# Kernel optimization log

Hardware: AMD Instinct MI355X
Metric: run time of the kernel (lower is better)

## Reference

```python
import jax, jax.numpy as jnp
import numpy as np

EPS = 1e-8
NEG_INF = -jnp.inf


def setup_inputs() -> dict:
    key = jax.random.key(0)
    k1, k2, k3, k4 = jax.random.split(key, 4)
    B1, S1, B2, S2, H = 64, 128, 64, 128, 768
    x1 = jax.random.normal(k1, (B1, S1, H), dtype=jnp.float32)
    x2 = jax.random.normal(k2, (B2, S2, H), dtype=jnp.float32)
    mask1 = jax.random.randint(k3, (B1, S1), 0, 2).astype(jnp.int32)
    mask2 = jax.random.randint(k4, (B2, S2), 0, 2).astype(jnp.int32)
    # ensure at least one valid token per sequence
    mask1 = mask1.at[:, 0].set(1)
    mask2 = mask2.at[:, 0].set(1)
    return {"x1": x1, "mask1": mask1, "x2": x2, "mask2": mask2}


def _full_cosine(x1, x2):
    # x1: (B1,S1,H), x2: (B2,S2,H) -> sim: (B1,B2,S1,S2)
    n1 = jnp.linalg.norm(x1, axis=-1)  # (B1,S1)
    n2 = jnp.linalg.norm(x2, axis=-1)  # (B2,S2)
    dots = jnp.einsum('ash,bth->abst', x1, x2)
    denom = jnp.maximum(n1[:, None, :, None] * n2[None, :, None, :], EPS)
    return dots / denom


def _masked_mean(sim, mask, axis):
    m = mask.astype(bool)
    num = jnp.sum(jnp.where(m, sim, 0.0), axis=axis)
    den = jnp.sum(mask.astype(sim.dtype), axis=axis)
    return num / den


def reference(x1, mask1, x2, mask2):
    sim = _full_cosine(x1, x2)  # (B1,B2,S1,S2), unmasked cosine
    masked = jnp.where(mask1.astype(bool)[:, None, :, None], sim, NEG_INF)
    masked = jnp.where(mask2.astype(bool)[None, :, None, :], masked, NEG_INF)
    ind1 = jnp.argmax(masked, axis=-1)  # (B1,B2,S1): best x2 token per x1 token
    ind2 = jnp.argmax(masked, axis=-2)  # (B1,B2,S2): best x1 token per x2 token
    # gather unmasked cosine at the argmax indices (equivalent to recomputing
    # cosine on the gathered vectors as the torch code does)
    sim1 = jnp.take_along_axis(sim, ind1[..., None], axis=3)[..., 0]  # (B1,B2,S1)
    sim2 = jnp.take_along_axis(sim, ind2[..., None, :], axis=2)[..., 0, :]  # (B1,B2,S2)
    m1 = jnp.broadcast_to(mask1[:, None, :], sim1.shape)
    m2 = jnp.broadcast_to(mask2[None, :, :], sim2.shape)
    s1 = _masked_mean(sim1, m1, axis=-1)  # (B1,B2)
    s2 = _masked_mean(sim2, m2, axis=-1)  # (B1,B2)
    return (s1 + s2) / 2
```

## Files before the change

kernel.cpp:

```cpp
#include <hip/hip_runtime.h>
#include <hip/hip_bf16.h>

#define H_DIM 768
#define S_LEN 128
#define NT 12
#define MROWS 8192

typedef __attribute__((ext_vector_type(8))) short short8;
typedef __attribute__((ext_vector_type(4))) float f32x4;

__device__ __forceinline__ void gload_lds16(const void* g, void* l) {
  __builtin_amdgcn_global_load_lds(
      (const __attribute__((address_space(1))) unsigned int*)g,
      (__attribute__((address_space(3))) unsigned int*)l, 16, 0, 0);
}

__global__ __launch_bounds__(128) void prep_kernel(
    const int* __restrict__ mask1, const int* __restrict__ mask2,
    int* __restrict__ dest, int* __restrict__ cnts) {
  const int sq = blockIdx.x;
  const int* mask = (sq < 64) ? (mask1 + sq * S_LEN) : (mask2 + (sq - 64) * S_LEN);
  const int tid = threadIdx.x;
  const int lane = tid & 63, wv = tid >> 6;
  const int m = mask[tid] ? 1 : 0;
  const unsigned long long bal = __ballot(m);
  const int pre = __popcll(bal & ((1ull << lane) - 1ull));
  __shared__ int wsum[2];
  if (lane == 0) wsum[wv] = __popcll(bal);
  __syncthreads();
  const int base = (wv == 1) ? wsum[0] : 0;
  dest[sq * S_LEN + tid] = m ? (base + pre) : -1;
  if (tid == 0) cnts[sq] = wsum[0] + wsum[1];
}

__global__ __launch_bounds__(512) void scan_kernel(
    const int* __restrict__ cnts, int* __restrict__ off1, int* __restrict__ off2,
    unsigned* __restrict__ vbitsM, unsigned* __restrict__ vbitsN,
    int* __restrict__ dims) {
  __shared__ int so1[65], so2[65];
  const int tid = threadIdx.x;
  const int lane = tid & 63, wv = tid >> 6;
  if (tid < 128) {
    const int* cb = (wv == 0) ? cnts : (cnts + 64);
    const int np = (cb[lane] + 15) & ~15;
    int inc = np;
#pragma unroll
    for (int o = 1; o < 64; o <<= 1) {
      const int t = __shfl_up(inc, o);
      if (lane >= o) inc += t;
    }
    int* so = wv ? so2 : so1;
    so[lane] = inc - np;
    if (lane == 63) so[64] = inc;
  }
  __syncthreads();
  const int Mtot = so1[64], Ntot = so2[64];
  if (tid == 0) {
    const int Mpad = (Mtot + 127) & ~127, Npad = (Ntot + 127) & ~127;
    dims[0] = Mpad; dims[1] = Npad; dims[2] = Mpad >> 7; dims[3] = Npad >> 7;
  }
  if (tid < 65) { off1[tid] = so1[tid]; off2[tid] = so2[tid]; }
  unsigned bm = 0, bn = 0;
  const int r0 = tid * 16;
  if (r0 < Mtot) {
    int s = 0;
    while (so1[s + 1] <= r0) ++s;
    const int b0 = so1[s], nv = cnts[s];
#pragma unroll
    for (int k = 0; k < 16; ++k)
      if (r0 + k - b0 < nv) bm |= (1u << k);
  }
  if (r0 < Ntot) {
    int s = 0;
    while (so2[s + 1] <= r0) ++s;
    const int b0 = so2[s], nv = cnts[64 + s];
#pragma unroll
    for (int k = 0; k < 16; ++k)
      if (r0 + k - b0 < nv) bn |= (1u << k);
  }
  vbitsM[tid] = bm;
  vbitsN[tid] = bn;
}

__global__ __launch_bounds__(256) void normzero_kernel(
    const float* __restrict__ x1, const float* __restrict__ x2,
    const int* __restrict__ dest, const int* __restrict__ off1,
    const int* __restrict__ off2,
    const unsigned* __restrict__ vbitsM, const unsigned* __restrict__ vbitsN,
    const int* __restrict__ dims,
    unsigned short* __restrict__ xc1, unsigned short* __restrict__ xc2) {
  const int gid = blockIdx.x;
  const int tid = threadIdx.x;
  if (gid >= 16384) {
    const int row = gid - 16384;
    if (tid < 96) {
      const short8 z8 = (short8){0, 0, 0, 0, 0, 0, 0, 0};
      if (row < dims[0] && !((vbitsM[row >> 4] >> (row & 15)) & 1u))
        reinterpret_cast<short8*>(xc1 + (size_t)row * H_DIM)[tid] = z8;
      if (row < dims[1] && !((vbitsN[row >> 4] >> (row & 15)) & 1u))
        reinterpret_cast<short8*>(xc2 + (size_t)row * H_DIM)[tid] = z8;
    }
    return;
  }
  const int sg = gid >> 7, tok = gid & 127;
  const int d = dest[sg * S_LEN + tok];
  if (d < 0) return;
  const bool is1 = (gid < 8192);
  const float* row = is1 ? (x1 + (size_t)gid * H_DIM)
                         : (x2 + (size_t)(gid - 8192) * H_DIM);
  const int grow = (is1 ? off1[sg] : off2[sg - 64]) + d;
  unsigned short* orow = (is1 ? xc1 : xc2) + (size_t)grow * H_DIM;
  float4 v = make_float4(0.f, 0.f, 0.f, 0.f);
  float ss = 0.f;
  if (tid < 192) {
    v = reinterpret_cast<const float4*>(row)[tid];
    ss = v.x * v.x + v.y * v.y + v.z * v.z + v.w * v.w;
  }
#pragma unroll
  for (int o = 32; o > 0; o >>= 1) ss += __shfl_down(ss, o);
  __shared__ float ws[4];
  if ((tid & 63) == 0) ws[tid >> 6] = ss;
  __syncthreads();
  const float scale = 1.0f / sqrtf(ws[0] + ws[1] + ws[2] + ws[3]);
  if (tid < 192) {
    union { ushort4 u; __hip_bfloat16 h[4]; } o;
    o.h[0] = __float2bfloat16(v.x * scale);
    o.h[1] = __float2bfloat16(v.y * scale);
    o.h[2] = __float2bfloat16(v.z * scale);
    o.h[3] = __float2bfloat16(v.w * scale);
    reinterpret_cast<ushort4*>(orow)[tid] = o.u;
  }
}

__global__ __launch_bounds__(256, 4) void gemm_kernel(
    const unsigned short* __restrict__ xc1, const unsigned short* __restrict__ xc2,
    const unsigned* __restrict__ vbitsM, const unsigned* __restrict__ vbitsN,
    const int* __restrict__ dims,
    float* __restrict__ rowgranT, float* __restrict__ colgranT) {
  __shared__ __align__(16) unsigned short Al[128 * 64];
  __shared__ __align__(16) unsigned short Bl[128 * 64];
  const int Mt = dims[2], Nt = dims[3];
  const int bid = blockIdx.x;
  const int band = bid & 7;
  const int idx = bid >> 3;
  const int Ntb = (Nt + 7) >> 3;
  const int mt = idx / Ntb;
  const int nt = band * Ntb + (idx - mt * Ntb);
  if (mt >= Mt || nt >= Nt) return;
  const int tid = threadIdx.x;
  const int lane = tid & 63, w = tid >> 6;
  const int wm = w >> 1, wn = w & 1;
  const int g = lane >> 4, rl = lane & 15;
  const unsigned short* A0 = xc1 + (size_t)mt * 128 * H_DIM;
  const unsigned short* B0 = xc2 + (size_t)nt * 128 * H_DIM;

  f32x4 acc[4][4];
#pragma unroll
  for (int i = 0; i < 4; ++i)
#pragma unroll
    for (int j = 0; j < 4; ++j) acc[i][j] = (f32x4){0.f, 0.f, 0.f, 0.f};

  for (int t = 0; t < NT; ++t) {
    __syncthreads();
    const int k0 = t * 64;
#pragma unroll
    for (int q = 0; q < 4; ++q) {
      const int s = q * 256 + tid;
      const int row = s >> 3;
      const int cb = (s & 7) ^ (row & 7);
      gload_lds16(A0 + (size_t)row * H_DIM + k0 + cb * 8, Al + s * 8);
      gload_lds16(B0 + (size_t)row * H_DIM + k0 + cb * 8, Bl + s * 8);
    }
    __syncthreads();
#pragma unroll
    for (int kf = 0; kf < 2; ++kf) {
      const int slot = (kf * 4 + g) ^ (rl & 7);
      short8 av[4], bv[4];
#pragma unroll
      for (int i = 0; i < 4; ++i)
        av[i] = *reinterpret_cast<const short8*>(
            &Al[(wm * 64 + i * 16 + rl) * 64 + slot * 8]);
#pragma unroll
      for (int j = 0; j < 4; ++j)
        bv[j] = *reinterpret_cast<const short8*>(
            &Bl[(wn * 64 + j * 16 + rl) * 64 + slot * 8]);
      __builtin_amdgcn_s_setprio(1);
#pragma unroll
      for (int i = 0; i < 4; ++i)
#pragma unroll
        for (int j = 0; j < 4; ++j)
          acc[i][j] = __builtin_amdgcn_mfma_f32_16x16x32_bf16(
              av[i], bv[j], acc[i][j], 0, 0, 0);
      __builtin_amdgcn_s_setprio(0);
    }
  }

  unsigned bM[4], bN[4];
#pragma unroll
  for (int i = 0; i < 4; ++i) bM[i] = vbitsM[mt * 8 + wm * 4 + i];
#pragma unroll
  for (int j = 0; j < 4; ++j) bN[j] = vbitsN[nt * 8 + wn * 4 + j];

#pragma unroll
  for (int i = 0; i < 4; ++i)
#pragma unroll
    for (int j = 0; j < 4; ++j) {
      const unsigned cvb = bN[j];
#pragma unroll
      for (int r = 0; r < 4; ++r) {
        float pm = ((cvb >> rl) & 1u) ? acc[i][j][r] : -INFINITY;
#pragma unroll
        for (int o = 1; o < 16; o <<= 1) pm = fmaxf(pm, __shfl_xor(pm, o));
        if (rl == 0)
          rowgranT[(size_t)(nt * 8 + wn * 4 + j) * MROWS + mt * 128 + wm * 64 +
                   i * 16 + g * 4 + r] = pm;
      }
    }
#pragma unroll
  for (int i = 0; i < 4; ++i)
#pragma unroll
    for (int j = 0; j < 4; ++j) {
      const unsigned rvb = bM[i];
      float cm = -INFINITY;
#pragma unroll
      for (int r = 0; r < 4; ++r)
        if ((rvb >> (g * 4 + r)) & 1u) cm = fmaxf(cm, acc[i][j][r]);
      cm = fmaxf(cm, __shfl_xor(cm, 16));
      cm = fmaxf(cm, __shfl_xor(cm, 32));
      if (g == 0)
        colgranT[(size_t)(mt * 8 + wm * 4 + i) * MROWS + nt * 128 + wn * 64 +
                 j * 16 + rl] = cm;
    }
}

__global__ __launch_bounds__(128) void reduce_kernel(
    const float* __restrict__ rowgranT, const float* __restrict__ colgranT,
    const int* __restrict__ cnts, const int* __restrict__ off1,
    const int* __restrict__ off2, float* __restrict__ out) {
  const int a = blockIdx.x >> 6, b = blockIdx.x & 63;
  const int n1 = cnts[a], n2 = cnts[64 + b];
  const int o1 = off1[a], o2 = off2[b];
  const int g2s = o2 >> 4, g2n = (n2 + 15) >> 4;
  const int g1s = o1 >> 4, g1n = (n1 + 15) >> 4;
  const int tid = threadIdx.x;
  float v1 = 0.f, v2 = 0.f;
  if (tid < n1) {
    float mx = -INFINITY;
    for (int q = 0; q < g2n; ++q)
      mx = fmaxf(mx, rowgranT[(size_t)(g2s + q) * MROWS + o1 + tid]);
    v1 = mx;
  }
  if (tid < n2) {
    float mx = -INFINITY;
    for (int q = 0; q < g1n; ++q)
      mx = fmaxf(mx, colgranT[(size_t)(g1s + q) * MROWS + o2 + tid]);
    v2 = mx;
  }
#pragma unroll
  for (int o = 32; o > 0; o >>= 1) {
    v1 += __shfl_down(v1, o);
    v2 += __shfl_down(v2, o);
  }
  __shared__ float s1[2], s2[2];
  if ((tid & 63) == 0) { s1[tid >> 6] = v1; s2[tid >> 6] = v2; }
  __syncthreads();
  if (tid == 0)
    out[a * 64 + b] =
        0.5f * ((s1[0] + s1[1]) / (float)n1 + (s2[0] + s2[1]) / (float)n2);
}

extern "C" void kernel_launch(void* const* d_in, const int* in_sizes, int n_in,
                              void* d_out, int out_size, void* d_ws, size_t ws_size,
                              hipStream_t stream) {
  const float* x1 = (const float*)d_in[0];
  const int* mask1 = (const int*)d_in[1];
  const float* x2 = (const float*)d_in[2];
  const int* mask2 = (const int*)d_in[3];
  float* out = (float*)d_out;

  unsigned short* xc1 = (unsigned short*)d_ws;
  unsigned short* xc2 = xc1 + (size_t)8192 * H_DIM;
  float* rowgranT = (float*)(xc2 + (size_t)8192 * H_DIM);
  float* colgranT = rowgranT + (size_t)512 * MROWS;
  int* dest = (int*)(colgranT + (size_t)512 * MROWS);
  int* cnts = dest + 128 * S_LEN;
  int* off1 = cnts + 128;
  int* off2 = off1 + 65;
  unsigned* vbitsM = (unsigned*)(off2 + 65);
  unsigned* vbitsN = vbitsM + 512;
  int* dims = (int*)(vbitsN + 512);

  prep_kernel<<<128, 128, 0, stream>>>(mask1, mask2, dest, cnts);
  scan_kernel<<<1, 512, 0, stream>>>(cnts, off1, off2, vbitsM, vbitsN, dims);
  normzero_kernel<<<24576, 256, 0, stream>>>(x1, x2, dest, off1, off2, vbitsM,
                                             vbitsN, dims, xc1, xc2);
  gemm_kernel<<<4096, 256, 0, stream>>>(xc1, xc2, vbitsM, vbitsN, dims,
                                        rowgranT, colgranT);
  reduce_kernel<<<4096, 128, 0, stream>>>(rowgranT, colgranT, cnts, off1, off2,
                                          out);
}
```

Before: 92.46 us.

## Quantize normalized rows to int8 with per-row scales and use int8 MFMA

Each compacted row is now quantized to int8 using its max-abs value, and a per-row scale stores the cosine normalization. The GEMM runs i8 16x16x64 MFMAs on half-size LDS tiles and rescales the int32 accumulators to float before the masked max reductions. This aims to halve operand traffic and raise matrix throughput. The cost is reduced precision, which may change argmax choices between near-tied similarities.

```diff
diff --git a/kernel.cpp b/kernel.cpp
--- a/kernel.cpp
+++ b/kernel.cpp
@@ -6,8 +6,8 @@
 #define NT 12
 #define MROWS 8192
 
-typedef __attribute__((ext_vector_type(8))) short short8;
-typedef __attribute__((ext_vector_type(4))) float f32x4;
+typedef __attribute__((ext_vector_type(4))) int int4v;
+typedef __attribute__((ext_vector_type(2))) int int2v;
 
 __device__ __forceinline__ void gload_lds16(const void* g, void* l) {
   __builtin_amdgcn_global_load_lds(
@@ -88,17 +88,22 @@
     const int* __restrict__ off2,
     const unsigned* __restrict__ vbitsM, const unsigned* __restrict__ vbitsN,
     const int* __restrict__ dims,
-    unsigned short* __restrict__ xc1, unsigned short* __restrict__ xc2) {
+    signed char* __restrict__ xq1, signed char* __restrict__ xq2,
+    float* __restrict__ sc1, float* __restrict__ sc2) {
   const int gid = blockIdx.x;
   const int tid = threadIdx.x;
   if (gid >= 16384) {
     const int row = gid - 16384;
+    const bool zM = (row < dims[0]) && !((vbitsM[row >> 4] >> (row & 15)) & 1u);
+    const bool zN = (row < dims[1]) && !((vbitsN[row >> 4] >> (row & 15)) & 1u);
     if (tid < 96) {
-      const short8 z8 = (short8){0, 0, 0, 0, 0, 0, 0, 0};
-      if (row < dims[0] && !((vbitsM[row >> 4] >> (row & 15)) & 1u))
-        reinterpret_cast<short8*>(xc1 + (size_t)row * H_DIM)[tid] = z8;
-      if (row < dims[1] && !((vbitsN[row >> 4] >> (row & 15)) & 1u))
-        reinterpret_cast<short8*>(xc2 + (size_t)row * H_DIM)[tid] = z8;
+      const int2v z = (int2v){0, 0};
+      if (zM) reinterpret_cast<int2v*>(xq1 + (size_t)row * H_DIM)[tid] = z;
+      if (zN) reinterpret_cast<int2v*>(xq2 + (size_t)row * H_DIM)[tid] = z;
+    }
+    if (tid == 0) {
+      if (zM) sc1[row] = 0.f;
+      if (zN) sc2[row] = 0.f;
     }
     return;
   }
@@ -109,36 +114,46 @@
   const float* row = is1 ? (x1 + (size_t)gid * H_DIM)
                          : (x2 + (size_t)(gid - 8192) * H_DIM);
   const int grow = (is1 ? off1[sg] : off2[sg - 64]) + d;
-  unsigned short* orow = (is1 ? xc1 : xc2) + (size_t)grow * H_DIM;
+  signed char* xq = is1 ? xq1 : xq2;
+  float* scp = is1 ? sc1 : sc2;
   float4 v = make_float4(0.f, 0.f, 0.f, 0.f);
-  float ss = 0.f;
+  float ss = 0.f, ma = 0.f;
   if (tid < 192) {
     v = reinterpret_cast<const float4*>(row)[tid];
     ss = v.x * v.x + v.y * v.y + v.z * v.z + v.w * v.w;
-  }
-#pragma unroll
-  for (int o = 32; o > 0; o >>= 1) ss += __shfl_down(ss, o);
-  __shared__ float ws[4];
-  if ((tid & 63) == 0) ws[tid >> 6] = ss;
+    ma = fmaxf(fmaxf(fabsf(v.x), fabsf(v.y)), fmaxf(fabsf(v.z), fabsf(v.w)));
+  }
+#pragma unroll
+  for (int o = 32; o > 0; o >>= 1) {
+    ss += __shfl_down(ss, o);
+    ma = fmaxf(ma, __shfl_down(ma, o));
+  }
+  __shared__ float ws[4], wmx[4];
+  if ((tid & 63) == 0) { ws[tid >> 6] = ss; wmx[tid >> 6] = ma; }
   __syncthreads();
-  const float scale = 1.0f / sqrtf(ws[0] + ws[1] + ws[2] + ws[3]);
+  const float norm = sqrtf(ws[0] + ws[1] + ws[2] + ws[3]);
+  const float maxab = fmaxf(fmaxf(wmx[0], wmx[1]), fmaxf(wmx[2], wmx[3]));
+  const float qs = 127.0f / maxab;
   if (tid < 192) {
-    union { ushort4 u; __hip_bfloat16 h[4]; } o;
-    o.h[0] = __float2bfloat16(v.x * scale);
-    o.h[1] = __float2bfloat16(v.y * scale);
-    o.h[2] = __float2bfloat16(v.z * scale);
-    o.h[3] = __float2bfloat16(v.w * scale);
-    reinterpret_cast<ushort4*>(orow)[tid] = o.u;
-  }
+    const int q0 = __float2int_rn(v.x * qs);
+    const int q1 = __float2int_rn(v.y * qs);
+    const int q2 = __float2int_rn(v.z * qs);
+    const int q3 = __float2int_rn(v.w * qs);
+    const unsigned p = (q0 & 0xff) | ((q1 & 0xff) << 8) | ((q2 & 0xff) << 16) |
+                       ((unsigned)(q3 & 0xff) << 24);
+    reinterpret_cast<unsigned*>(xq + (size_t)grow * H_DIM)[tid] = p;
+  }
+  if (tid == 0) scp[grow] = maxab / (127.0f * norm);
 }
 
 __global__ __launch_bounds__(256, 4) void gemm_kernel(
-    const unsigned short* __restrict__ xc1, const unsigned short* __restrict__ xc2,
+    const signed char* __restrict__ xq1, const signed char* __restrict__ xq2,
+    const float* __restrict__ sc1, const float* __restrict__ sc2,
     const unsigned* __restrict__ vbitsM, const unsigned* __restrict__ vbitsN,
     const int* __restrict__ dims,
     float* __restrict__ rowgranT, float* __restrict__ colgranT) {
-  __shared__ __align__(16) unsigned short Al[128 * 64];
-  __shared__ __align__(16) unsigned short Bl[128 * 64];
+  __shared__ __align__(16) signed char Al[128 * 64];
+  __shared__ __align__(16) signed char Bl[128 * 64];
   const int Mt = dims[2], Nt = dims[3];
   const int bid = blockIdx.x;
   const int band = bid & 7;
@@ -151,49 +166,56 @@
   const int lane = tid & 63, w = tid >> 6;
   const int wm = w >> 1, wn = w & 1;
   const int g = lane >> 4, rl = lane & 15;
-  const unsigned short* A0 = xc1 + (size_t)mt * 128 * H_DIM;
-  const unsigned short* B0 = xc2 + (size_t)nt * 128 * H_DIM;
-
-  f32x4 acc[4][4];
+  const signed char* A0 = xq1 + (size_t)mt * 128 * H_DIM;
+  const signed char* B0 = xq2 + (size_t)nt * 128 * H_DIM;
+
+  int4v acc[4][4];
 #pragma unroll
   for (int i = 0; i < 4; ++i)
 #pragma unroll
-    for (int j = 0; j < 4; ++j) acc[i][j] = (f32x4){0.f, 0.f, 0.f, 0.f};
-
+    for (int j = 0; j < 4; ++j) acc[i][j] = (int4v){0, 0, 0, 0};
+
+  const int slot = g ^ ((rl & 3) ^ ((rl >> 2) & 3));
   for (int t = 0; t < NT; ++t) {
     __syncthreads();
     const int k0 = t * 64;
 #pragma unroll
-    for (int q = 0; q < 4; ++q) {
+    for (int q = 0; q < 2; ++q) {
       const int s = q * 256 + tid;
-      const int row = s >> 3;
-      const int cb = (s & 7) ^ (row & 7);
-      gload_lds16(A0 + (size_t)row * H_DIM + k0 + cb * 8, Al + s * 8);
-      gload_lds16(B0 + (size_t)row * H_DIM + k0 + cb * 8, Bl + s * 8);
+      const int row = s >> 2;
+      const int swz = (row & 3) ^ ((row >> 2) & 3);
+      const int cb = (s & 3) ^ swz;
+      gload_lds16(A0 + (size_t)row * H_DIM + k0 + cb * 16, Al + s * 16);
+      gload_lds16(B0 + (size_t)row * H_DIM + k0 + cb * 16, Bl + s * 16);
     }
     __syncthreads();
-#pragma unroll
-    for (int kf = 0; kf < 2; ++kf) {
-      const int slot = (kf * 4 + g) ^ (rl & 7);
-      short8 av[4], bv[4];
-#pragma unroll
-      for (int i = 0; i < 4; ++i)
-        av[i] = *reinterpret_cast<const short8*>(
-            &Al[(wm * 64 + i * 16 + rl) * 64 + slot * 8]);
+    int4v av[4], bv[4];
+#pragma unroll
+    for (int i = 0; i < 4; ++i)
+      av[i] = *reinterpret_cast<const int4v*>(
+          &Al[(wm * 64 + i * 16 + rl) * 64 + slot * 16]);
+#pragma unroll
+    for (int j = 0; j < 4; ++j)
+      bv[j] = *reinterpret_cast<const int4v*>(
+          &Bl[(wn * 64 + j * 16 + rl) * 64 + slot * 16]);
+    __builtin_amdgcn_s_setprio(1);
+#pragma unroll
+    for (int i = 0; i < 4; ++i)
 #pragma unroll
       for (int j = 0; j < 4; ++j)
-        bv[j] = *reinterpret_cast<const short8*>(
-            &Bl[(wn * 64 + j * 16 + rl) * 64 + slot * 8]);
-      __builtin_amdgcn_s_setprio(1);
-#pragma unroll
-      for (int i = 0; i < 4; ++i)
-#pragma unroll
-        for (int j = 0; j < 4; ++j)
-          acc[i][j] = __builtin_amdgcn_mfma_f32_16x16x32_bf16(
-              av[i], bv[j], acc[i][j], 0, 0, 0);
-      __builtin_amdgcn_s_setprio(0);
-    }
-  }
+        acc[i][j] = __builtin_amdgcn_mfma_i32_16x16x64_i8(
+            av[i], bv[j], acc[i][j], 0, 0, 0);
+    __builtin_amdgcn_s_setprio(0);
+  }
+
+  float scB[4], scA[4][4];
+#pragma unroll
+  for (int j = 0; j < 4; ++j) scB[j] = sc2[nt * 128 + wn * 64 + j * 16 + rl];
+#pragma unroll
+  for (int i = 0; i < 4; ++i)
+#pragma unroll
+    for (int r = 0; r < 4; ++r)
+      scA[i][r] = sc1[mt * 128 + wm * 64 + i * 16 + g * 4 + r];
 
   unsigned bM[4], bN[4];
 #pragma unroll
@@ -208,7 +230,8 @@
       const unsigned cvb = bN[j];
 #pragma unroll
       for (int r = 0; r < 4; ++r) {
-        float pm = ((cvb >> rl) & 1u) ? acc[i][j][r] : -INFINITY;
+        const float val = (float)acc[i][j][r] * scA[i][r] * scB[j];
+        float pm = ((cvb >> rl) & 1u) ? val : -INFINITY;
 #pragma unroll
         for (int o = 1; o < 16; o <<= 1) pm = fmaxf(pm, __shfl_xor(pm, o));
         if (rl == 0)
@@ -224,7 +247,8 @@
       float cm = -INFINITY;
 #pragma unroll
       for (int r = 0; r < 4; ++r)
-        if ((rvb >> (g * 4 + r)) & 1u) cm = fmaxf(cm, acc[i][j][r]);
+        if ((rvb >> (g * 4 + r)) & 1u)
+          cm = fmaxf(cm, (float)acc[i][j][r] * scA[i][r] * scB[j]);
       cm = fmaxf(cm, __shfl_xor(cm, 16));
       cm = fmaxf(cm, __shfl_xor(cm, 32));
       if (g == 0)
@@ -278,11 +302,13 @@
   const int* mask2 = (const int*)d_in[3];
   float* out = (float*)d_out;
 
-  unsigned short* xc1 = (unsigned short*)d_ws;
-  unsigned short* xc2 = xc1 + (size_t)8192 * H_DIM;
-  float* rowgranT = (float*)(xc2 + (size_t)8192 * H_DIM);
+  signed char* xq1 = (signed char*)d_ws;
+  signed char* xq2 = xq1 + (size_t)8192 * H_DIM;
+  float* rowgranT = (float*)(xq2 + (size_t)8192 * H_DIM);
   float* colgranT = rowgranT + (size_t)512 * MROWS;
-  int* dest = (int*)(colgranT + (size_t)512 * MROWS);
+  float* sc1 = colgranT + (size_t)512 * MROWS;
+  float* sc2 = sc1 + 8192;
+  int* dest = (int*)(sc2 + 8192);
   int* cnts = dest + 128 * S_LEN;
   int* off1 = cnts + 128;
   int* off2 = off1 + 65;
@@ -293,9 +319,9 @@
   prep_kernel<<<128, 128, 0, stream>>>(mask1, mask2, dest, cnts);
   scan_kernel<<<1, 512, 0, stream>>>(cnts, off1, off2, vbitsM, vbitsN, dims);
   normzero_kernel<<<24576, 256, 0, stream>>>(x1, x2, dest, off1, off2, vbitsM,
-                                             vbitsN, dims, xc1, xc2);
-  gemm_kernel<<<4096, 256, 0, stream>>>(xc1, xc2, vbitsM, vbitsN, dims,
-                                        rowgranT, colgranT);
+                                             vbitsN, dims, xq1, xq2, sc1, sc2);
+  gemm_kernel<<<4096, 256, 0, stream>>>(xq1, xq2, sc1, sc2, vbitsM, vbitsN,
+                                        dims, rowgranT, colgranT);
   reduce_kernel<<<4096, 128, 0, stream>>>(rowgranT, colgranT, cnts, off1, off2,
                                           out);
 }
```

Result: faster. 85.82 us (-7.2%).
